# Performance work log

Measured on AMD Instinct MI355X. Metric: run time of the kernel, lower is better.

The kernel has to match this reference:

```python
import jax, jax.numpy as jnp
import numpy as np
import math

N, NP, D, H, W, HEADS = 4, 1024, 256, 64, 64, 8
DH = D // HEADS


def _norm_coords(height, width):
    # (height*width, 2) with (x, y) in [0, 1], row-major flatten (y outer, x inner)
    y = jnp.linspace(0.0, 1.0, height)
    x = jnp.linspace(0.0, 1.0, width)
    yg, xg = jnp.meshgrid(y, x, indexing='ij')
    return jnp.stack([xg.reshape(-1), yg.reshape(-1)], axis=-1)


def _pos_enc(coords, dim):
    # coords: (P, 2) -> (P, dim); even slots sin(x*div), odd slots cos(y*div)
    div = jnp.exp(jnp.arange(0, dim, 2, dtype=coords.dtype) * (-math.log(10000.0) / dim))
    s = jnp.sin(coords[:, 0:1] * div)  # (P, dim/2)
    c = jnp.cos(coords[:, 1:2] * div)  # (P, dim/2)
    return jnp.stack([s, c], axis=-1).reshape(coords.shape[0], dim)


def setup_inputs() -> dict:
    key = jax.random.key(0)
    ks = jax.random.split(key, 10)
    sc = 1.0 / math.sqrt(D)
    return {
        "local_feat": jax.random.normal(ks[0], (N, NP, D), jnp.float32),
        "global_feat": jax.random.normal(ks[1], (N, D, H, W), jnp.float32),
        "Wq": jax.random.normal(ks[2], (D, D), jnp.float32) * sc,
        "bq": jax.random.normal(ks[3], (D,), jnp.float32) * sc,
        "Wk": jax.random.normal(ks[4], (D, D), jnp.float32) * sc,
        "bk": jax.random.normal(ks[5], (D,), jnp.float32) * sc,
        "Wv": jax.random.normal(ks[6], (D, D), jnp.float32) * sc,
        "bv": jax.random.normal(ks[7], (D,), jnp.float32) * sc,
        "Wo": jax.random.normal(ks[8], (D, D), jnp.float32) * sc,
        "bo": jax.random.normal(ks[9], (D,), jnp.float32) * sc,
    }


def reference(local_feat, global_feat, Wq, bq, Wk, bk, Wv, bv, Wo, bo):
    n, N_p, d = local_feat.shape
    _, _, h, w = global_feat.shape
    hw = h * w
    P = int(math.sqrt(N_p))

    gf = jnp.transpose(global_feat.reshape(n, d, hw), (0, 2, 1))  # (n, HW, d)

    lf = local_feat + _pos_enc(_norm_coords(P, P), d)[None]       # (n, N_p, d)
    gf = gf + _pos_enc(_norm_coords(h, w), d)[None]               # (n, HW, d)

    q = (lf @ Wq.T + bq).reshape(n, N_p, HEADS, DH)
    k = (gf @ Wk.T + bk).reshape(n, hw, HEADS, DH)
    v = (gf @ Wv.T + bv).reshape(n, hw, HEADS, DH)

    scores = jnp.einsum('bqhd,bkhd->bhqk', q, k) / math.sqrt(DH)  # (n, H, N_p, HW)
    attn = jax.nn.softmax(scores, axis=-1)
    out = jnp.einsum('bhqk,bkhd->bqhd', attn, v).reshape(n, N_p, d)

    return (lf + out) @ Wo.T + bo
```

## Files before the change

kernel.cpp:

```cpp
#include <hip/hip_runtime.h>
#include <hip/hip_bf16.h>
#include <math.h>

#define NB    4
#define NPTS  1024
#define DD    256
#define HWW   4096
#define NHEAD 8
#define DHD   32
#define VTROW 4128

typedef short s8v  __attribute__((ext_vector_type(8)));
typedef float f4v  __attribute__((ext_vector_type(4)));
typedef unsigned int u2v __attribute__((ext_vector_type(2)));
typedef unsigned int u4v __attribute__((ext_vector_type(4)));

#define MFMA_BF16 __builtin_amdgcn_mfma_f32_16x16x32_bf16

#define PE_FACT (-9.210340371976184f / 256.0f)
#define QSCALE 0.2550348637f

__device__ __forceinline__ unsigned packbf(float hi, float lo) {
    return __builtin_amdgcn_perm(__float_as_uint(hi), __float_as_uint(lo), 0x07060302u);
}

__global__ __launch_bounds__(256) void prep(const float* __restrict__ lf,
                                            const float* __restrict__ gfeat,
                                            const float* __restrict__ wq,
                                            const float* __restrict__ wk,
                                            const float* __restrict__ wv,
                                            const float* __restrict__ wo,
                                            __hip_bfloat16* __restrict__ lf_pe_b,
                                            __hip_bfloat16* __restrict__ gf_pe_b,
                                            __hip_bfloat16* __restrict__ W4) {
    __shared__ float tile[32][33];
    int b = blockIdx.x, tid = threadIdx.x;
    if (b < 4096) {
        int idx = b * 256 + tid;
        int c = idx & 255, p = (idx >> 8) & 1023;
        float div = __expf((float)(c & ~1) * PE_FACT);
        float pe = (c & 1) ? __cosf((float)(p >> 5) * (1.0f / 31.0f) * div)
                           : __sinf((float)(p & 31) * (1.0f / 31.0f) * div);
        lf_pe_b[idx] = __float2bfloat16(lf[idx] + pe);
    } else if (b < 8192) {
        int t = b - 4096;
        int n = t >> 10, r = t & 1023;
        int p0 = (r >> 3) * 32, c0 = (r & 7) * 32;
        int tx = tid & 31, ty = tid >> 5;
#pragma unroll
        for (int i = 0; i < 4; ++i)
            tile[ty + 8 * i][tx] = gfeat[((size_t)n * DD + (c0 + ty + 8 * i)) * HWW + p0 + tx];
        __syncthreads();
#pragma unroll
        for (int i = 0; i < 4; ++i) {
            int p = p0 + ty + 8 * i, c = c0 + tx;
            float div = __expf((float)(c & ~1) * PE_FACT);
            float pe = (c & 1) ? __cosf((float)(p >> 6) * (1.0f / 63.0f) * div)
                               : __sinf((float)(p & 63) * (1.0f / 63.0f) * div);
            gf_pe_b[((size_t)n * HWW + p) * DD + c] = __float2bfloat16(tile[tx][ty + 8 * i] + pe);
        }
    } else {
        int idx = (b - 8192) * 256 + tid;
        int m = idx >> 16, r = idx & 65535;
        const float* src = (m == 0) ? wq : (m == 1) ? wk : (m == 2) ? wv : wo;
        W4[idx] = __float2bfloat16(src[r]);
    }
}

__global__ __launch_bounds__(256, 2) void gemmQKV(const __hip_bfloat16* __restrict__ Aq,
                                                  const __hip_bfloat16* __restrict__ Akv,
                                                  const __hip_bfloat16* __restrict__ W4,
                                                  const float* __restrict__ bq,
                                                  const float* __restrict__ bk,
                                                  const float* __restrict__ bv,
                                                  __hip_bfloat16* __restrict__ Qb,
                                                  __hip_bfloat16* __restrict__ Kb,
                                                  __hip_bfloat16* __restrict__ Vtb) {
    __shared__ __align__(16) unsigned shbuf[2304];
    int tid = threadIdx.x;
    int wave = tid >> 6, lane = tid & 63;
    int quad = lane >> 4, c16 = lane & 15;
    int b = blockIdx.x;

    int typ, c0, mgrp, mstride;
    const short* Ap;
    const short* Wp;
    const float* bias;
    if (b < 128) {
        typ = 0; c0 = (b >> 5) * 64; mgrp = b & 31; mstride = 2048;
        Ap = (const short*)Aq; Wp = (const short*)W4; bias = bq;
    } else {
        int bb = b - 128;
        int combo = bb >> 7;
        mgrp = bb & 127; mstride = 8192;
        int mat = combo & 1;
        typ = 1 + mat;
        c0 = (combo >> 1) * 64;
        Ap = (const short*)Akv;
        Wp = (const short*)W4 + (1 + mat) * DD * DD;
        bias = mat ? bv : bk;
    }

    s8v w[8][4];
    const short* wp0 = Wp + (c0 + c16) * DD + quad * 8;
#pragma unroll
    for (int ks = 0; ks < 8; ++ks)
#pragma unroll
        for (int t = 0; t < 4; ++t)
            w[ks][t] = *(const s8v*)(wp0 + t * 16 * DD + ks * 32);
    float bvv[4];
#pragma unroll
    for (int t = 0; t < 4; ++t) bvv[t] = bias[c0 + t * 16 + c16];

    int mbase0 = mgrp * 64;
    int mbase1 = mbase0 + mstride;
    const short* ap0 = Ap + (mbase0 + wave * 16 + c16) * DD + quad * 8;
    const short* ap1 = Ap + (mbase1 + wave * 16 + c16) * DD + quad * 8;
    s8v a0[8], a1[8];
#pragma unroll
    for (int ks = 0; ks < 8; ++ks) a0[ks] = *(const s8v*)(ap0 + ks * 32);
#pragma unroll
    for (int ks = 0; ks < 8; ++ks) a1[ks] = *(const s8v*)(ap1 + ks * 32);

#pragma unroll
    for (int it = 0; it < 2; ++it) {
        int mbase = it ? mbase1 : mbase0;
        f4v acc[4];
#pragma unroll
        for (int t = 0; t < 4; ++t) acc[t] = (f4v){0.f, 0.f, 0.f, 0.f};
#pragma unroll
        for (int ks = 0; ks < 8; ++ks) {
            s8v a = it ? a1[ks] : a0[ks];
#pragma unroll
            for (int t = 0; t < 4; ++t)
                acc[t] = MFMA_BF16(a, w[ks][t], acc[t], 0, 0, 0);
        }

        if (typ != 2) {
            short* kt = (short*)shbuf;
            __syncthreads();
#pragma unroll
            for (int t = 0; t < 4; ++t) {
#pragma unroll
                for (int r = 0; r < 4; ++r) {
                    float v = acc[t][r] + bvv[t];
                    if (typ == 0) v *= QSCALE;
                    __hip_bfloat16 hv = __float2bfloat16(v);
                    kt[(wave * 16 + quad * 4 + r) * 72 + t * 16 + c16] = *(short*)&hv;
                }
            }
            __syncthreads();
            int pl  = tid >> 2;
            int seg = tid & 3;
            const short* src = kt + pl * 72 + seg * 16;
            u4v w0 = *(const u4v*)(src);
            u4v w1 = *(const u4v*)(src + 8);
            int h   = (c0 >> 5) + (seg >> 1);
            int dh0 = (seg & 1) * 16;
            short* dst;
            if (typ == 0) {
                int row = mbase + pl;
                int n = row >> 10, p = row & 1023;
                dst = (short*)Qb + (((size_t)(n * NHEAD + h) << 10) + p) * DHD + dh0;
            } else {
                int n = mbase >> 12, p = (mbase & 4095) + pl;
                dst = (short*)Kb + (((size_t)(n * NHEAD + h) << 12) + p) * DHD + dh0;
            }
            *(u4v*)(dst)     = w0;
            *(u4v*)(dst + 8) = w1;
        } else {
            unsigned (*stv)[36] = (unsigned (*)[36])shbuf;
            __syncthreads();
#pragma unroll
            for (int t = 0; t < 4; ++t) {
#pragma unroll
                for (int rp = 0; rp < 2; ++rp) {
                    __hip_bfloat16 lo = __float2bfloat16(acc[t][2 * rp] + bvv[t]);
                    __hip_bfloat16 hi = __float2bfloat16(acc[t][2 * rp + 1] + bvv[t]);
                    unsigned dw = (unsigned)*(unsigned short*)&lo |
                                  ((unsigned)*(unsigned short*)&hi << 16);
                    stv[t * 16 + c16][wave * 8 + quad * 2 + rp] = dw;
                }
            }
            __syncthreads();
            int col = tid >> 2;
            int kd  = (tid & 3) * 8;
            int grp = kd & 16;
            int ob  = kd & 15;
            unsigned vals[8];
#pragma unroll
            for (int i = 0; i < 8; ++i) {
                int o = ob + i;
                int idw = ((o >> 2) << 1) | (o & 1) | ((o & 2) << 2);
                vals[i] = stv[col][grp + idw];
            }
            int nblk = mbase >> 12;
            int kb   = mbase & 4095;
            int gh = (c0 + col) >> 5, gdh = (c0 + col) & 31;
            short* vp = (short*)Vtb + ((size_t)(nblk * NHEAD + gh) * DHD + gdh) * VTROW + kb + kd * 2;
            *(u4v*)(vp)     = (u4v){vals[0], vals[1], vals[2], vals[3]};
            *(u4v*)(vp + 8) = (u4v){vals[4], vals[5], vals[6], vals[7]};
        }
    }
}

template <int NC>
__global__ __launch_bounds__(256) void attn(const __hip_bfloat16* __restrict__ Q,
                                            const __hip_bfloat16* __restrict__ Kg,
                                            const __hip_bfloat16* __restrict__ Vt,
                                            __hip_bfloat16* __restrict__ Opart,
                                            float* __restrict__ lpart) {
    constexpr int CK = HWW / NC;
    constexpr int NSTEP = CK / 32;

    int tid = threadIdx.x;
    int wave = tid >> 6, lane = tid & 63;
    int quad = lane >> 4, c16 = lane & 15;

    int id = blockIdx.x;
    int xcd = id & 7;
    int s = id >> 3;
    int qtile = s & 3;
    int gidx = ((s >> 2) << 3) | xcd;
    int bh = gidx & 31;
    int chunk = gidx >> 5;

    int q0 = qtile * 256 + wave * 64;

    const short* Qs = (const short*)Q + (size_t)bh * NPTS * DHD;
    const short* Ks = (const short*)Kg + ((size_t)bh * HWW + (size_t)chunk * CK) * DHD;
    const short* Vs = (const short*)Vt + (size_t)bh * DHD * VTROW + (size_t)chunk * CK;

    s8v aq[4];
#pragma unroll
    for (int g = 0; g < 4; ++g)
        aq[g] = *(const s8v*)(Qs + (q0 + g * 16 + c16) * DHD + quad * 8);

    const f4v zf = {0.f, 0.f, 0.f, 0.f};
    f4v o[4][2];
#pragma unroll
    for (int g = 0; g < 4; ++g) { o[g][0] = zf; o[g][1] = zf; }
    float lsum[4] = {0.f, 0.f, 0.f, 0.f};

    const short* kbase  = Ks + c16 * DHD + quad * 8;
    const short* v0base = Vs + c16 * VTROW + quad * 8;
    const short* v1base = Vs + (16 + c16) * VTROW + quad * 8;

    s8v kfA = *(const s8v*)(kbase);
    s8v kfB = *(const s8v*)(kbase + 16 * DHD);
    s8v vfA = *(const s8v*)(v0base);
    s8v vfB = *(const s8v*)(v1base);

    for (int st = 0; st < NSTEP; ++st) {
        bool more = (st + 1) < NSTEP;
        s8v nkA, nkB, nvA, nvB;
        if (more) {
            int ko = (st + 1) * 32;
            nkA = *(const s8v*)(kbase + ko * DHD);
            nkB = *(const s8v*)(kbase + ko * DHD + 16 * DHD);
            nvA = *(const s8v*)(v0base + ko);
            nvB = *(const s8v*)(v1base + ko);
        }
#pragma unroll
        for (int g = 0; g < 4; ++g) {
            f4v sA = MFMA_BF16(kfA, aq[g], zf, 0, 0, 0);
            f4v sB = MFMA_BF16(kfB, aq[g], zf, 0, 0, 0);
            float pA0 = __builtin_amdgcn_exp2f(sA[0]);
            float pA1 = __builtin_amdgcn_exp2f(sA[1]);
            float pA2 = __builtin_amdgcn_exp2f(sA[2]);
            float pA3 = __builtin_amdgcn_exp2f(sA[3]);
            float pB0 = __builtin_amdgcn_exp2f(sB[0]);
            float pB1 = __builtin_amdgcn_exp2f(sB[1]);
            float pB2 = __builtin_amdgcn_exp2f(sB[2]);
            float pB3 = __builtin_amdgcn_exp2f(sB[3]);
            lsum[g] += ((pA0 + pA1) + (pA2 + pA3)) + ((pB0 + pB1) + (pB2 + pB3));
            union { u4v u; s8v s; } pf;
            pf.u = (u4v){packbf(pA1, pA0), packbf(pA3, pA2),
                         packbf(pB1, pB0), packbf(pB3, pB2)};
            o[g][0] = MFMA_BF16(vfA, pf.s, o[g][0], 0, 0, 0);
            o[g][1] = MFMA_BF16(vfB, pf.s, o[g][1], 0, 0, 0);
        }
        if (more) { kfA = nkA; kfB = nkB; vfA = nvA; vfB = nvB; }
    }

    size_t obase = (size_t)(chunk * 32 + bh) * NPTS;
#pragma unroll
    for (int g = 0; g < 4; ++g) {
        float l = lsum[g];
        l += __shfl_xor(l, 16);
        l += __shfl_xor(l, 32);
        int q = q0 + g * 16 + c16;
        if (quad == 0) lpart[obase + q] = l;
        unsigned d0 = packbf(o[g][0][1], o[g][0][0]);
        unsigned d1 = packbf(o[g][0][3], o[g][0][2]);
        unsigned d2 = packbf(o[g][1][1], o[g][1][0]);
        unsigned d3 = packbf(o[g][1][3], o[g][1][2]);
        unsigned* op = (unsigned*)Opart + (obase + q) * (DHD / 2);
        *(u2v*)(op + 2 * quad)     = (u2v){d0, d1};
        *(u2v*)(op + 8 + 2 * quad) = (u2v){d2, d3};
    }
}

template <int NC>
__global__ __launch_bounds__(256) void combineO(const __hip_bfloat16* __restrict__ Opart,
                                                const float* __restrict__ lpart,
                                                const __hip_bfloat16* __restrict__ lf_pe,
                                                const __hip_bfloat16* __restrict__ Wo4,
                                                const float* __restrict__ bo,
                                                float* __restrict__ out) {
    __shared__ __align__(16) short al[16][264];
    int tid = threadIdx.x;
    int m0 = blockIdx.x * 16;
    {
        int rl  = tid >> 4;
        int seg = tid & 15;
        int h   = seg >> 1;
        int rg = m0 + rl;
        int n = rg >> 10, q = rg & 1023;
        size_t bhq = ((size_t)(n * NHEAD + h) << 10) + q;
        int dh0 = (seg & 1) * 16;
        float l = 0.f;
        float ov[16];
#pragma unroll
        for (int d = 0; d < 16; ++d) ov[d] = 0.f;
#pragma unroll
        for (int ch = 0; ch < NC; ++ch) {
            size_t base = (size_t)ch * 32 * NPTS + bhq;
            l += lpart[base];
            const unsigned* op = (const unsigned*)((const short*)Opart + base * DHD + dh0);
#pragma unroll
            for (int dw = 0; dw < 8; ++dw) {
                unsigned u = op[dw];
                ov[2 * dw]     += __uint_as_float(u << 16);
                ov[2 * dw + 1] += __uint_as_float(u & 0xffff0000u);
            }
        }
        float linv = 1.0f / l;
        const unsigned* lp = (const unsigned*)((const short*)lf_pe + ((size_t)rg * DD + seg * 16));
        unsigned* dst = (unsigned*)&al[rl][seg * 16];
#pragma unroll
        for (int dw = 0; dw < 8; ++dw) {
            unsigned u = lp[dw];
            float x0 = ov[2 * dw] * linv     + __uint_as_float(u << 16);
            float x1 = ov[2 * dw + 1] * linv + __uint_as_float(u & 0xffff0000u);
            dst[dw] = packbf(x1, x0);
        }
    }
    __syncthreads();
    int wave = tid >> 6, lane = tid & 63;
    int quad = lane >> 4, c16 = lane & 15;
    int ch0 = wave * 64;
    f4v acc[4];
#pragma unroll
    for (int t = 0; t < 4; ++t) acc[t] = (f4v){0.f, 0.f, 0.f, 0.f};
#pragma unroll
    for (int ks = 0; ks < 8; ++ks) {
        s8v af = *(const s8v*)&al[c16][ks * 32 + quad * 8];
#pragma unroll
        for (int t = 0; t < 4; ++t) {
            const short* wp = (const short*)Wo4 + (ch0 + t * 16 + c16) * DD + ks * 32 + quad * 8;
            s8v bf = *(const s8v*)wp;
            acc[t] = MFMA_BF16(af, bf, acc[t], 0, 0, 0);
        }
    }
#pragma unroll
    for (int t = 0; t < 4; ++t) {
        int col = ch0 + t * 16 + c16;
        float bv = bo[col];
#pragma unroll
        for (int r = 0; r < 4; ++r) {
            int row = m0 + quad * 4 + r;
            out[(size_t)row * DD + col] = acc[t][r] + bv;
        }
    }
}

extern "C" void kernel_launch(void* const* d_in, const int* in_sizes, int n_in,
                              void* d_out, int out_size, void* d_ws, size_t ws_size,
                              hipStream_t stream) {
    const float* lf    = (const float*)d_in[0];
    const float* gfeat = (const float*)d_in[1];
    const float* Wq    = (const float*)d_in[2];
    const float* bq    = (const float*)d_in[3];
    const float* Wk    = (const float*)d_in[4];
    const float* bk    = (const float*)d_in[5];
    const float* Wv    = (const float*)d_in[6];
    const float* bv    = (const float*)d_in[7];
    const float* Wo    = (const float*)d_in[8];
    const float* bo    = (const float*)d_in[9];

    const size_t MB = 1u << 20;
    char* ws = (char*)d_ws;
    __hip_bfloat16* lf_pe_b = (__hip_bfloat16*)(ws);
    __hip_bfloat16* gf_pe_b = (__hip_bfloat16*)(ws + 2 * MB);
    __hip_bfloat16* W4      = (__hip_bfloat16*)(ws + 10 * MB);
    __hip_bfloat16* Qb      = (__hip_bfloat16*)(ws + 10 * MB + 512 * 1024);
    __hip_bfloat16* Kb      = (__hip_bfloat16*)(ws + 12 * MB + 512 * 1024);
    __hip_bfloat16* Vtb     = (__hip_bfloat16*)(ws + 20 * MB + 512 * 1024);
    float*          lpart   = (float*)(ws + 31 * MB);
    __hip_bfloat16* Opart   = (__hip_bfloat16*)(ws + 32 * MB);

    prep<<<dim3(9216), dim3(256), 0, stream>>>(lf, gfeat, Wq, Wk, Wv, Wo,
                                               lf_pe_b, gf_pe_b, W4);
    gemmQKV<<<dim3(1152), dim3(256), 0, stream>>>(lf_pe_b, gf_pe_b, W4, bq, bk, bv,
                                                  Qb, Kb, Vtb);

    if (ws_size >= 48 * MB) {
        attn<8><<<dim3(128 * 8), dim3(256), 0, stream>>>(Qb, Kb, Vtb, Opart, lpart);
        combineO<8><<<dim3(256), dim3(256), 0, stream>>>(Opart, lpart, lf_pe_b,
                                                         W4 + 3 * DD * DD, bo, (float*)d_out);
    } else if (ws_size >= 40 * MB) {
        attn<4><<<dim3(128 * 4), dim3(256), 0, stream>>>(Qb, Kb, Vtb, Opart, lpart);
        combineO<4><<<dim3(256), dim3(256), 0, stream>>>(Opart, lpart, lf_pe_b,
                                                         W4 + 3 * DD * DD, bo, (float*)d_out);
    } else if (ws_size >= 36 * MB) {
        attn<2><<<dim3(128 * 2), dim3(256), 0, stream>>>(Qb, Kb, Vtb, Opart, lpart);
        combineO<2><<<dim3(256), dim3(256), 0, stream>>>(Opart, lpart, lf_pe_b,
                                                         W4 + 3 * DD * DD, bo, (float*)d_out);
    } else {
        attn<1><<<dim3(128 * 1), dim3(256), 0, stream>>>(Qb, Kb, Vtb, Opart, lpart);
        combineO<1><<<dim3(256), dim3(256), 0, stream>>>(Opart, lpart, lf_pe_b,
                                                         W4 + 3 * DD * DD, bo, (float*)d_out);
    }
}
```

Baseline: 159.5 us.

## Fuse all stages into one persistent kernel with software grid barriers

Merges the prep, QKV GEMM, attention and combine/output-projection kernels into a single persistent kernel of 512 blocks. Each stage loops over its work units with a grid-stride loop, and stages are separated by atomic-counter grid barriers whose counters are cleared by a memset before launch. This removes per-kernel launch gaps and tail effects. In exchange, the 512 blocks must all be co-resident or the barriers deadlock, and each stage now runs with fewer resident blocks than its original grid, which can reduce latency hiding. The attention split count is fixed at 8, and the old fallbacks for smaller workspaces are gone.

```diff
diff --git a/kernel.cpp b/kernel.cpp
--- a/kernel.cpp
+++ b/kernel.cpp
@@ -9,6 +9,8 @@
 #define NHEAD 8
 #define DHD   32
 #define VTROW 4128
+#define NC    8
+#define NBLK  512
 
 typedef short s8v  __attribute__((ext_vector_type(8)));
 typedef float f4v  __attribute__((ext_vector_type(4)));
@@ -24,353 +26,364 @@
     return __builtin_amdgcn_perm(__float_as_uint(hi), __float_as_uint(lo), 0x07060302u);
 }
 
-__global__ __launch_bounds__(256) void prep(const float* __restrict__ lf,
-                                            const float* __restrict__ gfeat,
-                                            const float* __restrict__ wq,
-                                            const float* __restrict__ wk,
-                                            const float* __restrict__ wv,
-                                            const float* __restrict__ wo,
-                                            __hip_bfloat16* __restrict__ lf_pe_b,
-                                            __hip_bfloat16* __restrict__ gf_pe_b,
-                                            __hip_bfloat16* __restrict__ W4) {
-    __shared__ float tile[32][33];
-    int b = blockIdx.x, tid = threadIdx.x;
-    if (b < 4096) {
-        int idx = b * 256 + tid;
-        int c = idx & 255, p = (idx >> 8) & 1023;
-        float div = __expf((float)(c & ~1) * PE_FACT);
-        float pe = (c & 1) ? __cosf((float)(p >> 5) * (1.0f / 31.0f) * div)
-                           : __sinf((float)(p & 31) * (1.0f / 31.0f) * div);
-        lf_pe_b[idx] = __float2bfloat16(lf[idx] + pe);
-    } else if (b < 8192) {
-        int t = b - 4096;
-        int n = t >> 10, r = t & 1023;
-        int p0 = (r >> 3) * 32, c0 = (r & 7) * 32;
-        int tx = tid & 31, ty = tid >> 5;
-#pragma unroll
-        for (int i = 0; i < 4; ++i)
-            tile[ty + 8 * i][tx] = gfeat[((size_t)n * DD + (c0 + ty + 8 * i)) * HWW + p0 + tx];
-        __syncthreads();
-#pragma unroll
-        for (int i = 0; i < 4; ++i) {
-            int p = p0 + ty + 8 * i, c = c0 + tx;
-            float div = __expf((float)(c & ~1) * PE_FACT);
-            float pe = (c & 1) ? __cosf((float)(p >> 6) * (1.0f / 63.0f) * div)
-                               : __sinf((float)(p & 63) * (1.0f / 63.0f) * div);
-            gf_pe_b[((size_t)n * HWW + p) * DD + c] = __float2bfloat16(tile[tx][ty + 8 * i] + pe);
-        }
-    } else {
-        int idx = (b - 8192) * 256 + tid;
-        int m = idx >> 16, r = idx & 65535;
-        const float* src = (m == 0) ? wq : (m == 1) ? wk : (m == 2) ? wv : wo;
-        W4[idx] = __float2bfloat16(src[r]);
+__device__ __forceinline__ void gridbar(unsigned* ctr, unsigned nb) {
+    __syncthreads();
+    if (threadIdx.x == 0) {
+        __threadfence();
+        __hip_atomic_fetch_add(ctr, 1u, __ATOMIC_RELEASE, __HIP_MEMORY_SCOPE_AGENT);
+        while (__hip_atomic_load(ctr, __ATOMIC_ACQUIRE, __HIP_MEMORY_SCOPE_AGENT) < nb)
+            __builtin_amdgcn_s_sleep(8);
     }
+    __syncthreads();
 }
 
-__global__ __launch_bounds__(256, 2) void gemmQKV(const __hip_bfloat16* __restrict__ Aq,
-                                                  const __hip_bfloat16* __restrict__ Akv,
-                                                  const __hip_bfloat16* __restrict__ W4,
-                                                  const float* __restrict__ bq,
-                                                  const float* __restrict__ bk,
-                                                  const float* __restrict__ bv,
-                                                  __hip_bfloat16* __restrict__ Qb,
-                                                  __hip_bfloat16* __restrict__ Kb,
-                                                  __hip_bfloat16* __restrict__ Vtb) {
-    __shared__ __align__(16) unsigned shbuf[2304];
+__global__ __launch_bounds__(256, 2) void mega(const float* __restrict__ lf,
+                                               const float* __restrict__ gfeat,
+                                               const float* __restrict__ wq,
+                                               const float* __restrict__ wk,
+                                               const float* __restrict__ wv,
+                                               const float* __restrict__ wo,
+                                               const float* __restrict__ bq,
+                                               const float* __restrict__ bk,
+                                               const float* __restrict__ bv,
+                                               const float* __restrict__ bo,
+                                               char* __restrict__ ws,
+                                               float* __restrict__ out) {
+    __shared__ __align__(16) char smem[9216];
+    const size_t MB = 1u << 20;
+    __hip_bfloat16* lf_pe_b = (__hip_bfloat16*)(ws);
+    __hip_bfloat16* gf_pe_b = (__hip_bfloat16*)(ws + 2 * MB);
+    __hip_bfloat16* W4      = (__hip_bfloat16*)(ws + 10 * MB);
+    __hip_bfloat16* Qb      = (__hip_bfloat16*)(ws + 10 * MB + 512 * 1024);
+    __hip_bfloat16* Kb      = (__hip_bfloat16*)(ws + 12 * MB + 512 * 1024);
+    __hip_bfloat16* Vtb     = (__hip_bfloat16*)(ws + 20 * MB + 512 * 1024);
+    unsigned*       barctr  = (unsigned*)(ws + 30 * MB);
+    float*          lpart   = (float*)(ws + 31 * MB);
+    __hip_bfloat16* Opart   = (__hip_bfloat16*)(ws + 32 * MB);
+
+    const unsigned nb = gridDim.x;
     int tid = threadIdx.x;
     int wave = tid >> 6, lane = tid & 63;
     int quad = lane >> 4, c16 = lane & 15;
-    int b = blockIdx.x;
-
-    int typ, c0, mgrp, mstride;
-    const short* Ap;
-    const short* Wp;
-    const float* bias;
-    if (b < 128) {
-        typ = 0; c0 = (b >> 5) * 64; mgrp = b & 31; mstride = 2048;
-        Ap = (const short*)Aq; Wp = (const short*)W4; bias = bq;
-    } else {
-        int bb = b - 128;
-        int combo = bb >> 7;
-        mgrp = bb & 127; mstride = 8192;
-        int mat = combo & 1;
-        typ = 1 + mat;
-        c0 = (combo >> 1) * 64;
-        Ap = (const short*)Akv;
-        Wp = (const short*)W4 + (1 + mat) * DD * DD;
-        bias = mat ? bv : bk;
-    }
-
-    s8v w[8][4];
-    const short* wp0 = Wp + (c0 + c16) * DD + quad * 8;
-#pragma unroll
-    for (int ks = 0; ks < 8; ++ks)
-#pragma unroll
-        for (int t = 0; t < 4; ++t)
-            w[ks][t] = *(const s8v*)(wp0 + t * 16 * DD + ks * 32);
-    float bvv[4];
-#pragma unroll
-    for (int t = 0; t < 4; ++t) bvv[t] = bias[c0 + t * 16 + c16];
-
-    int mbase0 = mgrp * 64;
-    int mbase1 = mbase0 + mstride;
-    const short* ap0 = Ap + (mbase0 + wave * 16 + c16) * DD + quad * 8;
-    const short* ap1 = Ap + (mbase1 + wave * 16 + c16) * DD + quad * 8;
-    s8v a0[8], a1[8];
-#pragma unroll
-    for (int ks = 0; ks < 8; ++ks) a0[ks] = *(const s8v*)(ap0 + ks * 32);
-#pragma unroll
-    for (int ks = 0; ks < 8; ++ks) a1[ks] = *(const s8v*)(ap1 + ks * 32);
-
-#pragma unroll
-    for (int it = 0; it < 2; ++it) {
-        int mbase = it ? mbase1 : mbase0;
-        f4v acc[4];
-#pragma unroll
-        for (int t = 0; t < 4; ++t) acc[t] = (f4v){0.f, 0.f, 0.f, 0.f};
-#pragma unroll
-        for (int ks = 0; ks < 8; ++ks) {
-            s8v a = it ? a1[ks] : a0[ks];
-#pragma unroll
-            for (int t = 0; t < 4; ++t)
-                acc[t] = MFMA_BF16(a, w[ks][t], acc[t], 0, 0, 0);
-        }
-
-        if (typ != 2) {
-            short* kt = (short*)shbuf;
-            __syncthreads();
-#pragma unroll
-            for (int t = 0; t < 4; ++t) {
-#pragma unroll
-                for (int r = 0; r < 4; ++r) {
-                    float v = acc[t][r] + bvv[t];
-                    if (typ == 0) v *= QSCALE;
-                    __hip_bfloat16 hv = __float2bfloat16(v);
-                    kt[(wave * 16 + quad * 4 + r) * 72 + t * 16 + c16] = *(short*)&hv;
-                }
-            }
-            __syncthreads();
-            int pl  = tid >> 2;
-            int seg = tid & 3;
-            const short* src = kt + pl * 72 + seg * 16;
-            u4v w0 = *(const u4v*)(src);
-            u4v w1 = *(const u4v*)(src + 8);
-            int h   = (c0 >> 5) + (seg >> 1);
-            int dh0 = (seg & 1) * 16;
-            short* dst;
-            if (typ == 0) {
-                int row = mbase + pl;
-                int n = row >> 10, p = row & 1023;
-                dst = (short*)Qb + (((size_t)(n * NHEAD + h) << 10) + p) * DHD + dh0;
+
+    {
+        float (*tile)[33] = (float (*)[33])smem;
+        for (int u = blockIdx.x; u < 9216; u += nb) {
+            if (u < 4096) {
+                int idx = u * 256 + tid;
+                int c = idx & 255, p = (idx >> 8) & 1023;
+                float div = __expf((float)(c & ~1) * PE_FACT);
+                float pe = (c & 1) ? __cosf((float)(p >> 5) * (1.0f / 31.0f) * div)
+                                   : __sinf((float)(p & 31) * (1.0f / 31.0f) * div);
+                lf_pe_b[idx] = __float2bfloat16(lf[idx] + pe);
+            } else if (u < 8192) {
+                int t = u - 4096;
+                int n = t >> 10, r = t & 1023;
+                int p0 = (r >> 3) * 32, c0 = (r & 7) * 32;
+                int tx = tid & 31, ty = tid >> 5;
+                __syncthreads();
+#pragma unroll
+                for (int i = 0; i < 4; ++i)
+                    tile[ty + 8 * i][tx] = gfeat[((size_t)n * DD + (c0 + ty + 8 * i)) * HWW + p0 + tx];
+                __syncthreads();
+#pragma unroll
+                for (int i = 0; i < 4; ++i) {
+                    int p = p0 + ty + 8 * i, c = c0 + tx;
+                    float div = __expf((float)(c & ~1) * PE_FACT);
+                    float pe = (c & 1) ? __cosf((float)(p >> 6) * (1.0f / 63.0f) * div)
+                                       : __sinf((float)(p & 63) * (1.0f / 63.0f) * div);
+                    gf_pe_b[((size_t)n * HWW + p) * DD + c] = __float2bfloat16(tile[tx][ty + 8 * i] + pe);
+                }
             } else {
-                int n = mbase >> 12, p = (mbase & 4095) + pl;
-                dst = (short*)Kb + (((size_t)(n * NHEAD + h) << 12) + p) * DHD + dh0;
-            }
-            *(u4v*)(dst)     = w0;
-            *(u4v*)(dst + 8) = w1;
-        } else {
-            unsigned (*stv)[36] = (unsigned (*)[36])shbuf;
-            __syncthreads();
-#pragma unroll
-            for (int t = 0; t < 4; ++t) {
-#pragma unroll
-                for (int rp = 0; rp < 2; ++rp) {
-                    __hip_bfloat16 lo = __float2bfloat16(acc[t][2 * rp] + bvv[t]);
-                    __hip_bfloat16 hi = __float2bfloat16(acc[t][2 * rp + 1] + bvv[t]);
-                    unsigned dw = (unsigned)*(unsigned short*)&lo |
-                                  ((unsigned)*(unsigned short*)&hi << 16);
-                    stv[t * 16 + c16][wave * 8 + quad * 2 + rp] = dw;
-                }
-            }
-            __syncthreads();
-            int col = tid >> 2;
-            int kd  = (tid & 3) * 8;
-            int grp = kd & 16;
-            int ob  = kd & 15;
-            unsigned vals[8];
-#pragma unroll
-            for (int i = 0; i < 8; ++i) {
-                int o = ob + i;
-                int idw = ((o >> 2) << 1) | (o & 1) | ((o & 2) << 2);
-                vals[i] = stv[col][grp + idw];
-            }
-            int nblk = mbase >> 12;
-            int kb   = mbase & 4095;
-            int gh = (c0 + col) >> 5, gdh = (c0 + col) & 31;
-            short* vp = (short*)Vtb + ((size_t)(nblk * NHEAD + gh) * DHD + gdh) * VTROW + kb + kd * 2;
-            *(u4v*)(vp)     = (u4v){vals[0], vals[1], vals[2], vals[3]};
-            *(u4v*)(vp + 8) = (u4v){vals[4], vals[5], vals[6], vals[7]};
+                int idx = (u - 8192) * 256 + tid;
+                int m = idx >> 16, r = idx & 65535;
+                const float* src = (m == 0) ? wq : (m == 1) ? wk : (m == 2) ? wv : wo;
+                W4[idx] = __float2bfloat16(src[r]);
+            }
         }
     }
-}
-
-template <int NC>
-__global__ __launch_bounds__(256) void attn(const __hip_bfloat16* __restrict__ Q,
-                                            const __hip_bfloat16* __restrict__ Kg,
-                                            const __hip_bfloat16* __restrict__ Vt,
-                                            __hip_bfloat16* __restrict__ Opart,
-                                            float* __restrict__ lpart) {
-    constexpr int CK = HWW / NC;
-    constexpr int NSTEP = CK / 32;
-
-    int tid = threadIdx.x;
-    int wave = tid >> 6, lane = tid & 63;
-    int quad = lane >> 4, c16 = lane & 15;
-
-    int id = blockIdx.x;
-    int xcd = id & 7;
-    int s = id >> 3;
-    int qtile = s & 3;
-    int gidx = ((s >> 2) << 3) | xcd;
-    int bh = gidx & 31;
-    int chunk = gidx >> 5;
-
-    int q0 = qtile * 256 + wave * 64;
-
-    const short* Qs = (const short*)Q + (size_t)bh * NPTS * DHD;
-    const short* Ks = (const short*)Kg + ((size_t)bh * HWW + (size_t)chunk * CK) * DHD;
-    const short* Vs = (const short*)Vt + (size_t)bh * DHD * VTROW + (size_t)chunk * CK;
-
-    s8v aq[4];
-#pragma unroll
-    for (int g = 0; g < 4; ++g)
-        aq[g] = *(const s8v*)(Qs + (q0 + g * 16 + c16) * DHD + quad * 8);
-
-    const f4v zf = {0.f, 0.f, 0.f, 0.f};
-    f4v o[4][2];
-#pragma unroll
-    for (int g = 0; g < 4; ++g) { o[g][0] = zf; o[g][1] = zf; }
-    float lsum[4] = {0.f, 0.f, 0.f, 0.f};
-
-    const short* kbase  = Ks + c16 * DHD + quad * 8;
-    const short* v0base = Vs + c16 * VTROW + quad * 8;
-    const short* v1base = Vs + (16 + c16) * VTROW + quad * 8;
-
-    s8v kfA = *(const s8v*)(kbase);
-    s8v kfB = *(const s8v*)(kbase + 16 * DHD);
-    s8v vfA = *(const s8v*)(v0base);
-    s8v vfB = *(const s8v*)(v1base);
-
-    for (int st = 0; st < NSTEP; ++st) {
-        bool more = (st + 1) < NSTEP;
-        s8v nkA, nkB, nvA, nvB;
-        if (more) {
-            int ko = (st + 1) * 32;
-            nkA = *(const s8v*)(kbase + ko * DHD);
-            nkB = *(const s8v*)(kbase + ko * DHD + 16 * DHD);
-            nvA = *(const s8v*)(v0base + ko);
-            nvB = *(const s8v*)(v1base + ko);
-        }
-#pragma unroll
-        for (int g = 0; g < 4; ++g) {
-            f4v sA = MFMA_BF16(kfA, aq[g], zf, 0, 0, 0);
-            f4v sB = MFMA_BF16(kfB, aq[g], zf, 0, 0, 0);
-            float pA0 = __builtin_amdgcn_exp2f(sA[0]);
-            float pA1 = __builtin_amdgcn_exp2f(sA[1]);
-            float pA2 = __builtin_amdgcn_exp2f(sA[2]);
-            float pA3 = __builtin_amdgcn_exp2f(sA[3]);
-            float pB0 = __builtin_amdgcn_exp2f(sB[0]);
-            float pB1 = __builtin_amdgcn_exp2f(sB[1]);
-            float pB2 = __builtin_amdgcn_exp2f(sB[2]);
-            float pB3 = __builtin_amdgcn_exp2f(sB[3]);
-            lsum[g] += ((pA0 + pA1) + (pA2 + pA3)) + ((pB0 + pB1) + (pB2 + pB3));
-            union { u4v u; s8v s; } pf;
-            pf.u = (u4v){packbf(pA1, pA0), packbf(pA3, pA2),
-                         packbf(pB1, pB0), packbf(pB3, pB2)};
-            o[g][0] = MFMA_BF16(vfA, pf.s, o[g][0], 0, 0, 0);
-            o[g][1] = MFMA_BF16(vfB, pf.s, o[g][1], 0, 0, 0);
-        }
-        if (more) { kfA = nkA; kfB = nkB; vfA = nvA; vfB = nvB; }
-    }
-
-    size_t obase = (size_t)(chunk * 32 + bh) * NPTS;
-#pragma unroll
-    for (int g = 0; g < 4; ++g) {
-        float l = lsum[g];
-        l += __shfl_xor(l, 16);
-        l += __shfl_xor(l, 32);
-        int q = q0 + g * 16 + c16;
-        if (quad == 0) lpart[obase + q] = l;
-        unsigned d0 = packbf(o[g][0][1], o[g][0][0]);
-        unsigned d1 = packbf(o[g][0][3], o[g][0][2]);
-        unsigned d2 = packbf(o[g][1][1], o[g][1][0]);
-        unsigned d3 = packbf(o[g][1][3], o[g][1][2]);
-        unsigned* op = (unsigned*)Opart + (obase + q) * (DHD / 2);
-        *(u2v*)(op + 2 * quad)     = (u2v){d0, d1};
-        *(u2v*)(op + 8 + 2 * quad) = (u2v){d2, d3};
-    }
-}
-
-template <int NC>
-__global__ __launch_bounds__(256) void combineO(const __hip_bfloat16* __restrict__ Opart,
-                                                const float* __restrict__ lpart,
-                                                const __hip_bfloat16* __restrict__ lf_pe,
-                                                const __hip_bfloat16* __restrict__ Wo4,
-                                                const float* __restrict__ bo,
-                                                float* __restrict__ out) {
-    __shared__ __align__(16) short al[16][264];
-    int tid = threadIdx.x;
-    int m0 = blockIdx.x * 16;
+    gridbar(barctr + 0, nb);
+
     {
-        int rl  = tid >> 4;
-        int seg = tid & 15;
-        int h   = seg >> 1;
-        int rg = m0 + rl;
-        int n = rg >> 10, q = rg & 1023;
-        size_t bhq = ((size_t)(n * NHEAD + h) << 10) + q;
-        int dh0 = (seg & 1) * 16;
-        float l = 0.f;
-        float ov[16];
-#pragma unroll
-        for (int d = 0; d < 16; ++d) ov[d] = 0.f;
-#pragma unroll
-        for (int ch = 0; ch < NC; ++ch) {
-            size_t base = (size_t)ch * 32 * NPTS + bhq;
-            l += lpart[base];
-            const unsigned* op = (const unsigned*)((const short*)Opart + base * DHD + dh0);
-#pragma unroll
-            for (int dw = 0; dw < 8; ++dw) {
-                unsigned u = op[dw];
-                ov[2 * dw]     += __uint_as_float(u << 16);
-                ov[2 * dw + 1] += __uint_as_float(u & 0xffff0000u);
-            }
-        }
-        float linv = 1.0f / l;
-        const unsigned* lp = (const unsigned*)((const short*)lf_pe + ((size_t)rg * DD + seg * 16));
-        unsigned* dst = (unsigned*)&al[rl][seg * 16];
-#pragma unroll
-        for (int dw = 0; dw < 8; ++dw) {
-            unsigned u = lp[dw];
-            float x0 = ov[2 * dw] * linv     + __uint_as_float(u << 16);
-            float x1 = ov[2 * dw + 1] * linv + __uint_as_float(u & 0xffff0000u);
-            dst[dw] = packbf(x1, x0);
+        for (int u = blockIdx.x; u < 1152; u += nb) {
+            int typ, c0, mgrp, mstride;
+            const short* Ap;
+            const short* Wp;
+            const float* bias;
+            if (u < 128) {
+                typ = 0; c0 = (u >> 5) * 64; mgrp = u & 31; mstride = 2048;
+                Ap = (const short*)lf_pe_b; Wp = (const short*)W4; bias = bq;
+            } else {
+                int bb = u - 128;
+                int combo = bb >> 7;
+                mgrp = bb & 127; mstride = 8192;
+                int mat = combo & 1;
+                typ = 1 + mat;
+                c0 = (combo >> 1) * 64;
+                Ap = (const short*)gf_pe_b;
+                Wp = (const short*)W4 + (1 + mat) * DD * DD;
+                bias = mat ? bv : bk;
+            }
+
+            s8v w[8][4];
+            const short* wp0 = Wp + (c0 + c16) * DD + quad * 8;
+#pragma unroll
+            for (int ks = 0; ks < 8; ++ks)
+#pragma unroll
+                for (int t = 0; t < 4; ++t)
+                    w[ks][t] = *(const s8v*)(wp0 + t * 16 * DD + ks * 32);
+            float bvv[4];
+#pragma unroll
+            for (int t = 0; t < 4; ++t) bvv[t] = bias[c0 + t * 16 + c16];
+
+            int mbase0 = mgrp * 64;
+            int mbase1 = mbase0 + mstride;
+            const short* ap0 = Ap + (mbase0 + wave * 16 + c16) * DD + quad * 8;
+            const short* ap1 = Ap + (mbase1 + wave * 16 + c16) * DD + quad * 8;
+            s8v a0[8], a1[8];
+#pragma unroll
+            for (int ks = 0; ks < 8; ++ks) a0[ks] = *(const s8v*)(ap0 + ks * 32);
+#pragma unroll
+            for (int ks = 0; ks < 8; ++ks) a1[ks] = *(const s8v*)(ap1 + ks * 32);
+
+#pragma unroll
+            for (int it = 0; it < 2; ++it) {
+                int mbase = it ? mbase1 : mbase0;
+                f4v acc[4];
+#pragma unroll
+                for (int t = 0; t < 4; ++t) acc[t] = (f4v){0.f, 0.f, 0.f, 0.f};
+#pragma unroll
+                for (int ks = 0; ks < 8; ++ks) {
+                    s8v a = it ? a1[ks] : a0[ks];
+#pragma unroll
+                    for (int t = 0; t < 4; ++t)
+                        acc[t] = MFMA_BF16(a, w[ks][t], acc[t], 0, 0, 0);
+                }
+
+                if (typ != 2) {
+                    short* kt = (short*)smem;
+                    __syncthreads();
+#pragma unroll
+                    for (int t = 0; t < 4; ++t) {
+#pragma unroll
+                        for (int r = 0; r < 4; ++r) {
+                            float v = acc[t][r] + bvv[t];
+                            if (typ == 0) v *= QSCALE;
+                            __hip_bfloat16 hv = __float2bfloat16(v);
+                            kt[(wave * 16 + quad * 4 + r) * 72 + t * 16 + c16] = *(short*)&hv;
+                        }
+                    }
+                    __syncthreads();
+                    int pl  = tid >> 2;
+                    int seg = tid & 3;
+                    const short* src = kt + pl * 72 + seg * 16;
+                    u4v w0 = *(const u4v*)(src);
+                    u4v w1 = *(const u4v*)(src + 8);
+                    int h   = (c0 >> 5) + (seg >> 1);
+                    int dh0 = (seg & 1) * 16;
+                    short* dst;
+                    if (typ == 0) {
+                        int row = mbase + pl;
+                        int n = row >> 10, p = row & 1023;
+                        dst = (short*)Qb + (((size_t)(n * NHEAD + h) << 10) + p) * DHD + dh0;
+                    } else {
+                        int n = mbase >> 12, p = (mbase & 4095) + pl;
+                        dst = (short*)Kb + (((size_t)(n * NHEAD + h) << 12) + p) * DHD + dh0;
+                    }
+                    *(u4v*)(dst)     = w0;
+                    *(u4v*)(dst + 8) = w1;
+                } else {
+                    unsigned (*stv)[36] = (unsigned (*)[36])smem;
+                    __syncthreads();
+#pragma unroll
+                    for (int t = 0; t < 4; ++t) {
+#pragma unroll
+                        for (int rp = 0; rp < 2; ++rp) {
+                            __hip_bfloat16 lo = __float2bfloat16(acc[t][2 * rp] + bvv[t]);
+                            __hip_bfloat16 hi = __float2bfloat16(acc[t][2 * rp + 1] + bvv[t]);
+                            unsigned dw = (unsigned)*(unsigned short*)&lo |
+                                          ((unsigned)*(unsigned short*)&hi << 16);
+                            stv[t * 16 + c16][wave * 8 + quad * 2 + rp] = dw;
+                        }
+                    }
+                    __syncthreads();
+                    int col = tid >> 2;
+                    int kd  = (tid & 3) * 8;
+                    int grp = kd & 16;
+                    int ob  = kd & 15;
+                    unsigned vals[8];
+#pragma unroll
+                    for (int i = 0; i < 8; ++i) {
+                        int o = ob + i;
+                        int idw = ((o >> 2) << 1) | (o & 1) | ((o & 2) << 2);
+                        vals[i] = stv[col][grp + idw];
+                    }
+                    int nblk = mbase >> 12;
+                    int kb   = mbase & 4095;
+                    int gh = (c0 + col) >> 5, gdh = (c0 + col) & 31;
+                    short* vp = (short*)Vtb + ((size_t)(nblk * NHEAD + gh) * DHD + gdh) * VTROW + kb + kd * 2;
+                    *(u4v*)(vp)     = (u4v){vals[0], vals[1], vals[2], vals[3]};
+                    *(u4v*)(vp + 8) = (u4v){vals[4], vals[5], vals[6], vals[7]};
+                }
+            }
         }
     }
-    __syncthreads();
-    int wave = tid >> 6, lane = tid & 63;
-    int quad = lane >> 4, c16 = lane & 15;
-    int ch0 = wave * 64;
-    f4v acc[4];
-#pragma unroll
-    for (int t = 0; t < 4; ++t) acc[t] = (f4v){0.f, 0.f, 0.f, 0.f};
-#pragma unroll
-    for (int ks = 0; ks < 8; ++ks) {
-        s8v af = *(const s8v*)&al[c16][ks * 32 + quad * 8];
-#pragma unroll
-        for (int t = 0; t < 4; ++t) {
-            const short* wp = (const short*)Wo4 + (ch0 + t * 16 + c16) * DD + ks * 32 + quad * 8;
-            s8v bf = *(const s8v*)wp;
-            acc[t] = MFMA_BF16(af, bf, acc[t], 0, 0, 0);
+    gridbar(barctr + 1, nb);
+
+    {
+        constexpr int CK = HWW / NC;
+        constexpr int NSTEP = CK / 32;
+        for (int u = blockIdx.x; u < 128 * NC; u += nb) {
+            int xcd = u & 7;
+            int s = u >> 3;
+            int qtile = s & 3;
+            int gidx = ((s >> 2) << 3) | xcd;
+            int bh = gidx & 31;
+            int chunk = gidx >> 5;
+            int q0 = qtile * 256 + wave * 64;
+
+            const short* Qs = (const short*)Qb + (size_t)bh * NPTS * DHD;
+            const short* Ks = (const short*)Kb + ((size_t)bh * HWW + (size_t)chunk * CK) * DHD;
+            const short* Vs = (const short*)Vtb + (size_t)bh * DHD * VTROW + (size_t)chunk * CK;
+
+            s8v aq[4];
+#pragma unroll
+            for (int g = 0; g < 4; ++g)
+                aq[g] = *(const s8v*)(Qs + (q0 + g * 16 + c16) * DHD + quad * 8);
+
+            const f4v zf = {0.f, 0.f, 0.f, 0.f};
+            f4v o[4][2];
+#pragma unroll
+            for (int g = 0; g < 4; ++g) { o[g][0] = zf; o[g][1] = zf; }
+            float lsum[4] = {0.f, 0.f, 0.f, 0.f};
+
+            const short* kbase  = Ks + c16 * DHD + quad * 8;
+            const short* v0base = Vs + c16 * VTROW + quad * 8;
+            const short* v1base = Vs + (16 + c16) * VTROW + quad * 8;
+
+            s8v kfA = *(const s8v*)(kbase);
+            s8v kfB = *(const s8v*)(kbase + 16 * DHD);
+            s8v vfA = *(const s8v*)(v0base);
+            s8v vfB = *(const s8v*)(v1base);
+
+            for (int st = 0; st < NSTEP; ++st) {
+                bool more = (st + 1) < NSTEP;
+                s8v nkA, nkB, nvA, nvB;
+                if (more) {
+                    int ko = (st + 1) * 32;
+                    nkA = *(const s8v*)(kbase + ko * DHD);
+                    nkB = *(const s8v*)(kbase + ko * DHD + 16 * DHD);
+                    nvA = *(const s8v*)(v0base + ko);
+                    nvB = *(const s8v*)(v1base + ko);
+                }
+#pragma unroll
+                for (int g = 0; g < 4; ++g) {
+                    f4v sA = MFMA_BF16(kfA, aq[g], zf, 0, 0, 0);
+                    f4v sB = MFMA_BF16(kfB, aq[g], zf, 0, 0, 0);
+                    float pA0 = __builtin_amdgcn_exp2f(sA[0]);
+                    float pA1 = __builtin_amdgcn_exp2f(sA[1]);
+                    float pA2 = __builtin_amdgcn_exp2f(sA[2]);
+                    float pA3 = __builtin_amdgcn_exp2f(sA[3]);
+                    float pB0 = __builtin_amdgcn_exp2f(sB[0]);
+                    float pB1 = __builtin_amdgcn_exp2f(sB[1]);
+                    float pB2 = __builtin_amdgcn_exp2f(sB[2]);
+                    float pB3 = __builtin_amdgcn_exp2f(sB[3]);
+                    lsum[g] += ((pA0 + pA1) + (pA2 + pA3)) + ((pB0 + pB1) + (pB2 + pB3));
+                    union { u4v uu; s8v ss; } pf;
+                    pf.uu = (u4v){packbf(pA1, pA0), packbf(pA3, pA2),
+                                  packbf(pB1, pB0), packbf(pB3, pB2)};
+                    o[g][0] = MFMA_BF16(vfA, pf.ss, o[g][0], 0, 0, 0);
+                    o[g][1] = MFMA_BF16(vfB, pf.ss, o[g][1], 0, 0, 0);
+                }
+                if (more) { kfA = nkA; kfB = nkB; vfA = nvA; vfB = nvB; }
+            }
+
+            size_t obase = (size_t)(chunk * 32 + bh) * NPTS;
+#pragma unroll
+            for (int g = 0; g < 4; ++g) {
+                float l = lsum[g];
+                l += __shfl_xor(l, 16);
+                l += __shfl_xor(l, 32);
+                int q = q0 + g * 16 + c16;
+                if (quad == 0) lpart[obase + q] = l;
+                unsigned d0 = packbf(o[g][0][1], o[g][0][0]);
+                unsigned d1 = packbf(o[g][0][3], o[g][0][2]);
+                unsigned d2 = packbf(o[g][1][1], o[g][1][0]);
+                unsigned d3 = packbf(o[g][1][3], o[g][1][2]);
+                unsigned* op = (unsigned*)Opart + (obase + q) * (DHD / 2);
+                *(u2v*)(op + 2 * quad)     = (u2v){d0, d1};
+                *(u2v*)(op + 8 + 2 * quad) = (u2v){d2, d3};
+            }
         }
     }
-#pragma unroll
-    for (int t = 0; t < 4; ++t) {
-        int col = ch0 + t * 16 + c16;
-        float bv = bo[col];
-#pragma unroll
-        for (int r = 0; r < 4; ++r) {
-            int row = m0 + quad * 4 + r;
-            out[(size_t)row * DD + col] = acc[t][r] + bv;
+    gridbar(barctr + 2, nb);
+
+    {
+        short (*al)[264] = (short (*)[264])smem;
+        for (int u = blockIdx.x; u < 256; u += nb) {
+            int m0 = u * 16;
+            __syncthreads();
+            {
+                int rl  = tid >> 4;
+                int seg = tid & 15;
+                int h   = seg >> 1;
+                int rg = m0 + rl;
+                int n = rg >> 10, q = rg & 1023;
+                size_t bhq = ((size_t)(n * NHEAD + h) << 10) + q;
+                int dh0 = (seg & 1) * 16;
+                float l = 0.f;
+                float ov[16];
+#pragma unroll
+                for (int d = 0; d < 16; ++d) ov[d] = 0.f;
+#pragma unroll
+                for (int ch = 0; ch < NC; ++ch) {
+                    size_t base = (size_t)ch * 32 * NPTS + bhq;
+                    l += lpart[base];
+                    const unsigned* op = (const unsigned*)((const short*)Opart + base * DHD + dh0);
+#pragma unroll
+                    for (int dw = 0; dw < 8; ++dw) {
+                        unsigned uu = op[dw];
+                        ov[2 * dw]     += __uint_as_float(uu << 16);
+                        ov[2 * dw + 1] += __uint_as_float(uu & 0xffff0000u);
+                    }
+                }
+                float linv = 1.0f / l;
+                const unsigned* lp = (const unsigned*)((const short*)lf_pe_b + ((size_t)rg * DD + seg * 16));
+                unsigned* dst = (unsigned*)&al[rl][seg * 16];
+#pragma unroll
+                for (int dw = 0; dw < 8; ++dw) {
+                    unsigned uu = lp[dw];
+                    float x0 = ov[2 * dw] * linv     + __uint_as_float(uu << 16);
+                    float x1 = ov[2 * dw + 1] * linv + __uint_as_float(uu & 0xffff0000u);
+                    dst[dw] = packbf(x1, x0);
+                }
+            }
+            __syncthreads();
+            const short* Wo4 = (const short*)(W4 + 3 * DD * DD);
+            int ch0 = wave * 64;
+            f4v acc[4];
+#pragma unroll
+            for (int t = 0; t < 4; ++t) acc[t] = (f4v){0.f, 0.f, 0.f, 0.f};
+#pragma unroll
+            for (int ks = 0; ks < 8; ++ks) {
+                s8v af = *(const s8v*)&al[c16][ks * 32 + quad * 8];
+#pragma unroll
+                for (int t = 0; t < 4; ++t) {
+                    const short* wp = Wo4 + (ch0 + t * 16 + c16) * DD + ks * 32 + quad * 8;
+                    s8v bf = *(const s8v*)wp;
+                    acc[t] = MFMA_BF16(af, bf, acc[t], 0, 0, 0);
+                }
+            }
+#pragma unroll
+            for (int t = 0; t < 4; ++t) {
+                int col = ch0 + t * 16 + c16;
+                float bv2 = bo[col];
+#pragma unroll
+                for (int r = 0; r < 4; ++r) {
+                    int row = m0 + quad * 4 + r;
+                    out[(size_t)row * DD + col] = acc[t][r] + bv2;
+                }
+            }
         }
     }
 }
@@ -388,38 +401,11 @@
     const float* bv    = (const float*)d_in[7];
     const float* Wo    = (const float*)d_in[8];
     const float* bo    = (const float*)d_in[9];
-
-    const size_t MB = 1u << 20;
-    char* ws = (char*)d_ws;
-    __hip_bfloat16* lf_pe_b = (__hip_bfloat16*)(ws);
-    __hip_bfloat16* gf_pe_b = (__hip_bfloat16*)(ws + 2 * MB);
-    __hip_bfloat16* W4      = (__hip_bfloat16*)(ws + 10 * MB);
-    __hip_bfloat16* Qb      = (__hip_bfloat16*)(ws + 10 * MB + 512 * 1024);
-    __hip_bfloat16* Kb      = (__hip_bfloat16*)(ws + 12 * MB + 512 * 1024);
-    __hip_bfloat16* Vtb     = (__hip_bfloat16*)(ws + 20 * MB + 512 * 1024);
-    float*          lpart   = (float*)(ws + 31 * MB);
-    __hip_bfloat16* Opart   = (__hip_bfloat16*)(ws + 32 * MB);
-
-    prep<<<dim3(9216), dim3(256), 0, stream>>>(lf, gfeat, Wq, Wk, Wv, Wo,
-                                               lf_pe_b, gf_pe_b, W4);
-    gemmQKV<<<dim3(1152), dim3(256), 0, stream>>>(lf_pe_b, gf_pe_b, W4, bq, bk, bv,
-                                                  Qb, Kb, Vtb);
-
-    if (ws_size >= 48 * MB) {
-        attn<8><<<dim3(128 * 8), dim3(256), 0, stream>>>(Qb, Kb, Vtb, Opart, lpart);
-        combineO<8><<<dim3(256), dim3(256), 0, stream>>>(Opart, lpart, lf_pe_b,
-                                                         W4 + 3 * DD * DD, bo, (float*)d_out);
-    } else if (ws_size >= 40 * MB) {
-        attn<4><<<dim3(128 * 4), dim3(256), 0, stream>>>(Qb, Kb, Vtb, Opart, lpart);
-        combineO<4><<<dim3(256), dim3(256), 0, stream>>>(Opart, lpart, lf_pe_b,
-                                                         W4 + 3 * DD * DD, bo, (float*)d_out);
-    } else if (ws_size >= 36 * MB) {
-        attn<2><<<dim3(128 * 2), dim3(256), 0, stream>>>(Qb, Kb, Vtb, Opart, lpart);
-        combineO<2><<<dim3(256), dim3(256), 0, stream>>>(Opart, lpart, lf_pe_b,
-                                                         W4 + 3 * DD * DD, bo, (float*)d_out);
-    } else {
-        attn<1><<<dim3(128 * 1), dim3(256), 0, stream>>>(Qb, Kb, Vtb, Opart, lpart);
-        combineO<1><<<dim3(256), dim3(256), 0, stream>>>(Opart, lpart, lf_pe_b,
-                                                         W4 + 3 * DD * DD, bo, (float*)d_out);
-    }
+    char*  wsp  = (char*)d_ws;
+    float* outp = (float*)d_out;
+
+    hipMemsetAsync(wsp + (30u << 20), 0, 256, stream);
+
+    mega<<<dim3(NBLK), dim3(256), 0, stream>>>(lf, gfeat, Wq, Wk, Wv, Wo,
+                                               bq, bk, bv, bo, wsp, outp);
 }
```

Measured after the change: 416.1 us. 2.61x slower.
